# Kernel tuning notes

Hardware: AMD Instinct MI355X
Metric: run time of the kernel (lower is better)

## Reference

```python
import jax, jax.numpy as jnp
import numpy as np

VOCAB = 128000; D = 128; H = 4; HD = D // H; NL = 2; DOUT = 64
MAXW = 32; B = 64; L = 64; N_ITERS = 32

def _ln(x, g, b):
    m = jnp.mean(x, -1, keepdims=True)
    v = jnp.var(x, -1, keepdims=True)
    return (x - m) * jax.lax.rsqrt(v + 1e-5) * g + b

def _encoder(x, pad, p):
    # post-norm torch TransformerEncoderLayer, relu activation. x: [N,W,D], pad True=padding key
    neg = jnp.where(pad, -1e9, 0.0)[:, None, None, :]
    n = x.shape[0]
    for l in range(NL):
        qkv = x @ p["Wqkv"][l].T + p["bqkv"][l]
        q, k, v = jnp.split(qkv, 3, axis=-1)
        q = q.reshape(n, MAXW, H, HD).transpose(0, 2, 1, 3)
        k = k.reshape(n, MAXW, H, HD).transpose(0, 2, 1, 3)
        v = v.reshape(n, MAXW, H, HD).transpose(0, 2, 1, 3)
        s = jnp.einsum('nhqd,nhkd->nhqk', q, k) * (1.0 / float(np.sqrt(HD))) + neg
        o = jnp.einsum('nhqk,nhkd->nhqd', jax.nn.softmax(s, -1), v)
        o = o.transpose(0, 2, 1, 3).reshape(n, MAXW, D) @ p["Wo"][l].T + p["bo"][l]
        x = _ln(x + o, p["ln1g"][l], p["ln1b"][l])
        f = jax.nn.relu(x @ p["W1"][l].T + p["b1"][l]) @ p["W2"][l].T + p["b2"][l]
        x = _ln(x + f, p["ln2g"][l], p["ln2b"][l])
    return x

def _forward(p, token_ids, padding_mask, key):
    seq_len = jnp.sum(~padding_mask, 1).astype(jnp.int32)
    pos_idx = jnp.arange(MAXW)
    bidx = jnp.arange(B)

    def _head(x, W1h, b1h, W2h, b2h):
        return (jax.nn.relu(x @ W1h.T + b1h) @ W2h.T + b2h)[:, 0]

    def _gru(x, h):
        gi = x @ p["gru_Wih"].T + p["gru_bih"]
        gh = h @ p["gru_Whh"].T + p["gru_bhh"]
        ir, iz, inn = jnp.split(gi, 3, -1)
        hr, hz, hn = jnp.split(gh, 3, -1)
        r = jax.nn.sigmoid(ir + hr)
        z = jax.nn.sigmoid(iz + hz)
        return (1.0 - z) * jnp.tanh(inn + r * hn) + z * h

    def step(carry, k):
        win_ids, win_len, input_pos, gru_h, done = carry
        active = ~done
        pad = ~((pos_idx[None, :] < win_len[:, None]) & active[:, None])
        pad = pad.at[:, 0].set(False)  # keep softmax finite for empty windows; t1 zeroed below
        x = p["tok_emb"][win_ids] + p["pos_emb"][None, :, :]
        enc = _encoder(x, pad, p)
        last = enc[bidx, jnp.maximum(win_len - 1, 0)]
        vec = last @ p["proj_W"].T + p["proj_b"]
        vec = vec / jnp.maximum(jnp.linalg.norm(vec, axis=-1, keepdims=True), 1e-12)
        nonempty = (win_len > 0) & active
        t1 = jnp.where(nonempty[:, None], vec, 0.0)
        gru_h = jnp.where(active[:, None], _gru(t1, gru_h), gru_h)
        has_input = active & (input_pos < seq_len)
        nt = token_ids[bidx, jnp.clip(input_pos, 0, L - 1)]
        next_embs = jnp.where(has_input[:, None], p["tok_emb"][nt], 0.0)
        acc_l = _head(jnp.concatenate([next_embs, t1, gru_h], 1), p["acc_W1"], p["acc_b1"], p["acc_W2"], p["acc_b2"])
        tg = jnp.concatenate([t1, gru_h], 1)
        emt_l = _head(tg, p["emt_W1"], p["emt_b1"], p["emt_W2"], p["emt_b2"])
        evt_l = _head(tg, p["evt_W1"], p["evt_b1"], p["evt_W2"], p["evt_b2"])
        k1, k2, k3 = jax.random.split(k, 3)
        acc_s = jax.random.bernoulli(k1, jax.nn.sigmoid(acc_l))
        emt_s = jax.random.bernoulli(k2, jax.nn.sigmoid(emt_l))
        evt_s = jax.random.bernoulli(k3, jax.nn.sigmoid(evt_l))
        lp = jnp.stack([jax.nn.log_sigmoid(jnp.where(acc_s, acc_l, -acc_l)),
                        jax.nn.log_sigmoid(jnp.where(emt_s, emt_l, -emt_l)),
                        jax.nn.log_sigmoid(jnp.where(evt_s, evt_l, -evt_l))], 1)
        dec = jnp.stack([acc_s, emt_s, evt_s], 1).astype(jnp.float32)
        a = acc_s & has_input
        e = emt_s & nonempty
        v = evt_s & nonempty
        none = active & ~(a | e | v)
        a = a | (none & has_input)
        e = e | (none & ~has_input & (win_len > 0))
        a_eff = a & (win_len < MAXW)
        win_ids = jnp.where(a_eff[:, None] & (pos_idx[None, :] == win_len[:, None]), nt[:, None], win_ids)
        input_pos = input_pos + a_eff.astype(jnp.int32)
        win_len = win_len + a_eff.astype(jnp.int32)
        emit_event = e & (win_len > 0)
        v_eff = v & (win_len > 0)
        win_ids = jnp.where(v_eff[:, None], jnp.roll(win_ids, -1, axis=1), win_ids)
        win_len = win_len - v_eff.astype(jnp.int32)
        done = done | (active & (input_pos >= seq_len) & (win_len == 0))
        return (win_ids, win_len, input_pos, gru_h, done), (t1, lp, dec, emit_event)

    init = (jnp.zeros((B, MAXW), dtype=token_ids.dtype), jnp.zeros(B, jnp.int32), jnp.zeros(B, jnp.int32),
            jnp.zeros((B, D), jnp.float32), seq_len == 0)
    keys = jax.random.split(key, N_ITERS)
    _, (t1s, lps, decs, emits) = jax.lax.scan(step, init, keys)
    return t1s, lps, decs, jnp.sum(emits.astype(jnp.int32), 0)

def setup_inputs():
    key = jax.random.key(0)
    ks = jax.random.split(key, 20)
    def rn(k, shape):
        return jax.random.normal(k, shape, jnp.float32) * 0.02
    inp = {}
    inp["token_ids"] = jax.random.randint(ks[0], (B, L), 0, VOCAB)
    inp["padding_mask"] = jnp.zeros((B, L), dtype=bool)
    inp["token_instr_idx"] = jax.random.randint(ks[1], (B, L), 0, 32)
    inp["n_instructions"] = jax.random.randint(ks[2], (B,), 1, 32)
    inp["tok_emb"] = rn(ks[3], (VOCAB, D))
    inp["pos_emb"] = rn(ks[4], (MAXW, D))
    inp["Wqkv"] = rn(ks[5], (NL, 3 * D, D)); inp["bqkv"] = jnp.zeros((NL, 3 * D))
    inp["Wo"] = rn(ks[6], (NL, D, D)); inp["bo"] = jnp.zeros((NL, D))
    inp["ln1g"] = jnp.ones((NL, D)); inp["ln1b"] = jnp.zeros((NL, D))
    inp["W1"] = rn(ks[7], (NL, 4 * D, D)); inp["b1"] = jnp.zeros((NL, 4 * D))
    inp["W2"] = rn(ks[8], (NL, D, 4 * D)); inp["b2"] = jnp.zeros((NL, D))
    inp["ln2g"] = jnp.ones((NL, D)); inp["ln2b"] = jnp.zeros((NL, D))
    inp["proj_W"] = rn(ks[9], (DOUT, D)); inp["proj_b"] = jnp.zeros((DOUT,))
    inp["gru_Wih"] = rn(ks[10], (3 * D, DOUT)); inp["gru_Whh"] = rn(ks[11], (3 * D, D))
    inp["gru_bih"] = jnp.zeros((3 * D,)); inp["gru_bhh"] = jnp.zeros((3 * D,))
    inp["acc_W1"] = rn(ks[12], (D, 2 * D + DOUT)); inp["acc_b1"] = jnp.zeros((D,))
    inp["acc_W2"] = rn(ks[13], (1, D)); inp["acc_b2"] = jnp.full((1,), 2.0)
    inp["emt_W1"] = rn(ks[14], (D, D + DOUT)); inp["emt_b1"] = jnp.zeros((D,))
    inp["emt_W2"] = rn(ks[15], (1, D)); inp["emt_b2"] = jnp.full((1,), -2.0)
    inp["evt_W1"] = rn(ks[16], (D, D + DOUT)); inp["evt_b1"] = jnp.zeros((D,))
    inp["evt_W2"] = rn(ks[17], (1, D)); inp["evt_b2"] = jnp.full((1,), -2.0)
    return inp

def reference(token_ids, padding_mask, token_instr_idx, n_instructions, tok_emb, pos_emb, Wqkv, bqkv, Wo, bo, ln1g, ln1b, W1, b1, W2, b2, ln2g, ln2b, proj_W, proj_b, gru_Wih, gru_Whh, gru_bih, gru_bhh, acc_W1, acc_b1, acc_W2, acc_b2, emt_W1, emt_b1, emt_W2, emt_b2, evt_W1, evt_b1, evt_W2, evt_b2):
    p = dict(tok_emb=tok_emb, pos_emb=pos_emb, Wqkv=Wqkv, bqkv=bqkv, Wo=Wo, bo=bo, ln1g=ln1g, ln1b=ln1b,
             W1=W1, b1=b1, W2=W2, b2=b2, ln2g=ln2g, ln2b=ln2b, proj_W=proj_W, proj_b=proj_b,
             gru_Wih=gru_Wih, gru_Whh=gru_Whh, gru_bih=gru_bih, gru_bhh=gru_bhh,
             acc_W1=acc_W1, acc_b1=acc_b1, acc_W2=acc_W2, acc_b2=acc_b2,
             emt_W1=emt_W1, emt_b1=emt_b1, emt_W2=emt_W2, emt_b2=emt_b2,
             evt_W1=evt_W1, evt_b1=evt_b1, evt_W2=evt_W2, evt_b2=evt_b2)
    # token_instr_idx / n_instructions are only used for emission bookkeeping (no tensor math); unused here.
    return _forward(p, token_ids, padding_mask, jax.random.key(42))
```

## Files before the change

### kernel.cpp

```cpp
#include <hip/hip_runtime.h>
#include <hip/hip_bf16.h>


#define XS 132
#define QS 388
#define HS 516
#define PS 36
#define VS 36
#define NW 16

struct KParams {
  const int* token_ids;
  const unsigned char* pad;
  const void *tok_emb, *pos_emb, *Wqkv, *bqkv, *Wo, *bo, *ln1g, *ln1b;
  const void *W1, *b1, *W2, *b2, *ln2g, *ln2b, *projW, *projb;
  const void *gWih, *gWhh, *gbih, *gbhh;
  const void *accW1, *accb1, *accW2, *accb2;
  const void *emtW1, *emtb1, *emtW2, *emtb2;
  const void *evtW1, *evtb1, *evtW2, *evtb2;
  float* out;
};

struct Smem {
  float xbuf[32 * XS];
  float qh[32 * HS];
  float obuf[32 * XS];
  float pbuf[4608];
  float vT[128 * VS];
  float attT[128];
  float tva[128];
  double gild[384];
  double ghld[384];
  double hsd[128];
  double t1d[64];
  double catd[320];
  double hid2d[384];
  double logitsd[3];
  int win_ids[32];
  int sI[6];
  unsigned keyts[32][2];
};

__device__ __forceinline__ float ldw(const float* p){ return *p; }
__device__ __forceinline__ float ldw(const unsigned short* p){
  return __uint_as_float(((unsigned)*p) << 16);
}
__device__ __forceinline__ float4 ld4(const float* p){ return *(const float4*)p; }
__device__ __forceinline__ float4 ld4(const unsigned short* p){
  ushort4 u = *(const ushort4*)p;
  return make_float4(__uint_as_float((unsigned)u.x << 16),
                     __uint_as_float((unsigned)u.y << 16),
                     __uint_as_float((unsigned)u.z << 16),
                     __uint_as_float((unsigned)u.w << 16));
}
template<typename WT>
__device__ __forceinline__ double ldwd(const WT* p){ return (double)ldw(p); }

__device__ __forceinline__ float temb(const void* te, int isb, long long idx){
  if (isb) return __uint_as_float(((unsigned)((const unsigned short*)te)[idx]) << 16);
  return ((const float*)te)[idx];
}

__device__ __forceinline__ void tfry(unsigned k0, unsigned k1, unsigned x0, unsigned x1,
                                     unsigned &o0, unsigned &o1){
  unsigned ks2 = k0 ^ k1 ^ 0x1BD11BDAu;
  unsigned x = x0 + k0, y = x1 + k1;
#define TFR(r) { x += y; y = (y << r) | (y >> (32 - r)); y ^= x; }
  TFR(13) TFR(15) TFR(26) TFR(6)  x += k1;  y += ks2 + 1u;
  TFR(17) TFR(29) TFR(16) TFR(24) x += ks2; y += k0 + 2u;
  TFR(13) TFR(15) TFR(26) TFR(6)  x += k0;  y += k1 + 3u;
  TFR(17) TFR(29) TFR(16) TFR(24) x += k1;  y += ks2 + 4u;
  TFR(13) TFR(15) TFR(26) TFR(6)  x += ks2; y += k0 + 5u;
#undef TFR
  o0 = x; o1 = y;
}
__device__ __forceinline__ float u01(unsigned bits){
  return __uint_as_float((bits >> 9) | 0x3f800000u) - 1.0f;
}
__device__ __forceinline__ double logsigd(double x){
  return fmin(x, 0.0) - log1p(exp(-fabs(x)));
}
__device__ __forceinline__ float wredsum(float v, int width){
  for (int m = width >> 1; m > 0; m >>= 1) v += __shfl_xor(v, m, width);
  return v;
}
__device__ __forceinline__ double wredsumd(double v, int width){
  for (int m = width >> 1; m > 0; m >>= 1) v += __shfl_xor(v, m, width);
  return v;
}
__device__ __forceinline__ float dot4f(float4 a, float4 b){
  return a.x*b.x + a.y*b.y + a.z*b.z + a.w*b.w;
}

template<int T, int K, bool RELU, int VOFF, typename WT>
__device__ void gemm_tok(const WT* __restrict__ Wm, const WT* __restrict__ bias,
                         int J, const float* __restrict__ xl, int xs,
                         float* __restrict__ ol, int os, int ntok,
                         int lane, int wv, int nwv, float* __restrict__ vt)
{
  const int JBG = J >> 6;
  const int ntt = (ntok + T - 1) / T;
  for (int item = wv; item < JBG * ntt; item += nwv) {
    const int jg = item % JBG, tt = item / JBG;
    const int j0 = jg * 64 + lane;
    float acc[T];
#pragma unroll
    for (int t = 0; t < T; ++t) acc[t] = 0.f;
    const float* xr = xl + tt * T * xs;
    const WT* wr = Wm + (size_t)j0 * K;
#pragma unroll 4
    for (int k = 0; k < K; k += 4) {
      float4 w = ld4(wr + k);
      float4 xv[T];
#pragma unroll
      for (int t = 0; t < T; ++t) xv[t] = *(const float4*)(xr + t * xs + k);
#pragma unroll
      for (int t = 0; t < T; ++t)
        acc[t] += w.x * xv[t].x + w.y * xv[t].y + w.z * xv[t].z + w.w * xv[t].w;
    }
    float bj = ldw(bias + j0);
#pragma unroll
    for (int t = 0; t < T; ++t) {
      int tok = tt * T + t;
      if (tok < ntok) {
        float v = acc[t] + bj;
        if (RELU) v = fmaxf(v, 0.f);
        if (VOFF >= 0 && j0 >= VOFF) vt[(j0 - VOFF) * VS + tok] = v;
        else                         ol[tok * os + j0] = v;
      }
    }
  }
}

template<int K, typename WT>
__device__ __forceinline__ float dotgf(const WT* __restrict__ w, const float* x){
  float acc = 0.f;
#pragma unroll 8
  for (int k = 0; k < K; k += 4) {
    float4 wv = ld4(w + k);
    acc += wv.x * x[k] + wv.y * x[k+1] + wv.z * x[k+2] + wv.w * x[k+3];
  }
  return acc;
}
template<int K, typename WT>
__device__ __forceinline__ double dotgd(const WT* __restrict__ w, const double* x){
  double acc = 0.0;
#pragma unroll 8
  for (int k = 0; k < K; k += 4) {
    float4 wv = ld4(w + k);
    acc += (double)wv.x * x[k] + (double)wv.y * x[k+1]
         + (double)wv.z * x[k+2] + (double)wv.w * x[k+3];
  }
  return acc;
}
template<int K, typename WT>
__device__ __forceinline__ double dotgdx(const WT* __restrict__ w, const float* x){
  double acc = 0.0;
#pragma unroll 8
  for (int k = 0; k < K; k += 4) {
    float4 wv = ld4(w + k);
    acc += (double)wv.x * (double)x[k] + (double)wv.y * (double)x[k+1]
         + (double)wv.z * (double)x[k+2] + (double)wv.w * (double)x[k+3];
  }
  return acc;
}

template<typename WT>
__device__ void ln_rows(float* xb, const float* ob, const WT* __restrict__ g,
                        const WT* __restrict__ bb, int W, int tid){
  if (tid >= 256) return;
  const int i = tid >> 3, sub = tid & 7;
  const int base = i * XS + sub * 16;
  float y[16];
  float s = 0.f;
#pragma unroll
  for (int u = 0; u < 16; u += 4) {
    float4 xv = *(const float4*)(xb + base + u);
    float4 ov = *(const float4*)(ob + base + u);
    y[u] = xv.x + ov.x; y[u+1] = xv.y + ov.y; y[u+2] = xv.z + ov.z; y[u+3] = xv.w + ov.w;
    s += y[u] + y[u+1] + y[u+2] + y[u+3];
  }
  s = wredsum(s, 8);
  const float m = s * (1.0f / 128.0f);
  float vs = 0.f;
#pragma unroll
  for (int u = 0; u < 16; ++u) { float d = y[u] - m; vs += d * d; }
  vs = wredsum(vs, 8);
  const float rstd = 1.0f / sqrtf(vs * (1.0f / 128.0f) + 1e-5f);
  if (i < W) {
#pragma unroll
    for (int u = 0; u < 16; u += 4) {
      float4 gg = ld4(g + sub * 16 + u);
      float4 bv = ld4(bb + sub * 16 + u);
      float4 r;
      r.x = (y[u]   - m) * rstd * gg.x + bv.x;
      r.y = (y[u+1] - m) * rstd * gg.y + bv.y;
      r.z = (y[u+2] - m) * rstd * gg.z + bv.z;
      r.w = (y[u+3] - m) * rstd * gg.w + bv.w;
      *(float4*)(xb + base + u) = r;
    }
  }
}
template<typename WT>
__device__ __forceinline__ void ln_tail(float* xrow, const float* add,
                                        const WT* __restrict__ g,
                                        const WT* __restrict__ bb, int tid){
  if (tid < 64) {
    float y0 = xrow[tid] + add[tid];
    float y1 = xrow[64 + tid] + add[64 + tid];
    float m = wredsum(y0 + y1, 64) * (1.0f / 128.0f);
    float d0 = y0 - m, d1 = y1 - m;
    float rstd = 1.0f / sqrtf(wredsum(d0 * d0 + d1 * d1, 64) * (1.0f / 128.0f) + 1e-5f);
    xrow[tid] = d0 * rstd * ldw(g + tid) + ldw(bb + tid);
    xrow[64 + tid] = d1 * rstd * ldw(g + 64 + tid) + ldw(bb + 64 + tid);
  }
}

template<typename WT>
__device__ void run_all(const KParams& P, Smem& S, int row, int tid, int isbEmb){
  const WT* tok_embw = (const WT*)P.tok_emb;
  const WT* pos_emb = (const WT*)P.pos_emb;
  const WT* Wqkv = (const WT*)P.Wqkv;   const WT* bqkv = (const WT*)P.bqkv;
  const WT* Wo = (const WT*)P.Wo;       const WT* bo = (const WT*)P.bo;
  const WT* ln1g = (const WT*)P.ln1g;   const WT* ln1b = (const WT*)P.ln1b;
  const WT* W1 = (const WT*)P.W1;       const WT* b1 = (const WT*)P.b1;
  const WT* W2 = (const WT*)P.W2;       const WT* b2 = (const WT*)P.b2;
  const WT* ln2g = (const WT*)P.ln2g;   const WT* ln2b = (const WT*)P.ln2b;
  const WT* projW = (const WT*)P.projW; const WT* projb = (const WT*)P.projb;
  const WT* gWih = (const WT*)P.gWih;   const WT* gWhh = (const WT*)P.gWhh;
  const WT* gbih = (const WT*)P.gbih;   const WT* gbhh = (const WT*)P.gbhh;
  const WT* accW1 = (const WT*)P.accW1; const WT* accb1 = (const WT*)P.accb1;
  const WT* accW2 = (const WT*)P.accW2; const WT* accb2 = (const WT*)P.accb2;
  const WT* emtW1 = (const WT*)P.emtW1; const WT* emtb1 = (const WT*)P.emtb1;
  const WT* emtW2 = (const WT*)P.emtW2; const WT* emtb2 = (const WT*)P.emtb2;
  const WT* evtW1 = (const WT*)P.evtW1; const WT* evtb1 = (const WT*)P.evtb1;
  const WT* evtW2 = (const WT*)P.evtW2; const WT* evtb2 = (const WT*)P.evtb2;

  const int lane = tid & 63, wid = tid >> 6;

  if (tid == 0) {
    int seq = 0;
    for (int l = 0; l < 64; ++l) seq += (P.pad[row * 64 + l] == 0);
    S.sI[0] = 0; S.sI[1] = 0; S.sI[2] = (seq == 0) ? 1 : 0; S.sI[3] = seq; S.sI[4] = 0;
  }
  if (tid < 128) S.hsd[tid] = 0.0;
  if (tid < 32) {
    S.win_ids[tid] = 0;
    unsigned a0, a1;
    tfry(0u, 42u, 0u, (unsigned)tid, a0, a1);
    S.keyts[tid][0] = a0; S.keyts[tid][1] = a1;
  }
  for (int idx = tid; idx < 128 * VS; idx += 1024) S.vT[idx] = 0.f;
  __syncthreads();

  for (int t = 0; t < 32; ++t) {
    const int wl = S.sI[0], ip = S.sI[1], done = S.sI[2], seq = S.sI[3];
    const int act = !done;
    const int W = wl;
    const int enc = (act && wl > 0) ? 1 : 0;
    const int jl = (W > 0) ? (W - 1) : 0;
    const int Wp4 = (W + 3) & ~3;

    if (enc) {
      for (int idx = tid; idx < W * 16; idx += 1024) {
        int i = idx >> 4, d0 = (idx & 15) << 3;
        const WT* te = tok_embw + (long long)S.win_ids[i] * 128 + d0;
        const WT* pe = pos_emb + (size_t)i * 128 + d0;
        float4 t0 = ld4(te), t1 = ld4(te + 4), p0 = ld4(pe), p1 = ld4(pe + 4);
        float* dst = &S.xbuf[i * XS + d0];
        float4 r0, r1;
        r0.x = t0.x + p0.x; r0.y = t0.y + p0.y; r0.z = t0.z + p0.z; r0.w = t0.w + p0.w;
        r1.x = t1.x + p1.x; r1.y = t1.y + p1.y; r1.z = t1.z + p1.z; r1.w = t1.w + p1.w;
        *(float4*)dst = r0;
        *(float4*)(dst + 4) = r1;
      }
      __syncthreads();
      gemm_tok<8, 128, false, 256>(Wqkv, bqkv, 384, S.xbuf, XS, S.qh, QS, W, lane, wid, NW, S.vT);
      __syncthreads();
      if (tid < 256) {
        int r = tid >> 1, half = tid & 1;
        int h = r >> 5, i = r & 31;
        if (i < W) {
          float4 q[8];
#pragma unroll
          for (int kk = 0; kk < 8; ++kk) q[kk] = *(const float4*)&S.qh[i * QS + h * 32 + kk * 4];
          const int pb = r * PS;
          const int j0 = half * 16;
          const int j1 = (j0 + 16 < W) ? (j0 + 16) : W;
          float m = -1e30f;
          for (int j = j0; j < j1; ++j) {
            float s = 0.f;
#pragma unroll
            for (int kk = 0; kk < 8; ++kk)
              s += dot4f(q[kk], *(const float4*)&S.qh[j * QS + 128 + h * 32 + kk * 4]);
            s *= 0.17677669529663687f;
            S.pbuf[pb + j] = s;
            m = fmaxf(m, s);
          }
          m = fmaxf(m, __shfl_xor(m, 1, 64));
          float sum = 0.f;
          for (int j = j0; j < j1; ++j) {
            float e = expf(S.pbuf[pb + j] - m);
            S.pbuf[pb + j] = e;
            sum += e;
          }
          sum += __shfl_xor(sum, 1, 64);
          float rs = 1.0f / sum;
          for (int j = j0; j < j1; ++j) S.pbuf[pb + j] *= rs;
          for (int j = W + half; j < Wp4; j += 2) S.pbuf[pb + j] = 0.f;
        }
      } else if (act) {
        int jj = tid - 256;
        int j = jj >> 1, h = jj & 1;
        double v = dotgd<64>(gWhh + (size_t)j * 128 + h * 64, S.hsd + h * 64);
        v += __shfl_xor(v, 1, 64);
        if (h == 0) S.ghld[j] = ldwd(gbhh + j) + v;
      }
      __syncthreads();
      {
        int c = tid & 127, g = tid >> 7;
        int h = c >> 5;
        const float* vrow = &S.vT[c * VS];
        for (int i = g; i < W; i += 8) {
          const float* prow = &S.pbuf[(h * 32 + i) * PS];
          float acc = 0.f;
          for (int j4 = 0; j4 < W; j4 += 4) {
            float4 p = *(const float4*)(prow + j4);
            float4 v = *(const float4*)(vrow + j4);
            acc += p.x * v.x + p.y * v.y + p.z * v.z + p.w * v.w;
          }
          S.obuf[i * XS + c] = acc;
        }
      }
      __syncthreads();
      gemm_tok<4, 128, false, -1>(Wo, bo, 128, S.obuf, XS, S.pbuf, XS, W, lane, wid, NW, S.vT);
      __syncthreads();
      ln_rows(S.xbuf, S.pbuf, ln1g, ln1b, W, tid);
      __syncthreads();
      gemm_tok<8, 128, true, -1>(W1, b1, 512, S.xbuf, XS, S.qh, HS, W, lane, wid, NW, S.vT);
      __syncthreads();
      gemm_tok<4, 512, false, -1>(W2, b2, 128, S.qh, HS, S.obuf, XS, W, lane, wid, NW, S.vT);
      __syncthreads();
      ln_rows(S.xbuf, S.obuf, ln2g, ln2b, W, tid);
      __syncthreads();
      {
        const WT* Wq = Wqkv + 384 * 128;
        const WT* bq = bqkv + 384;
        if (wid < 14) {
          gemm_tok<8, 128, false, 128>(Wq + 128 * 128, bq + 128, 256,
                                       S.xbuf, XS, S.qh + 128, QS, W, lane, wid, 14, S.vT);
        } else {
          int j = tid - 896;
          S.qh[jl * QS + j] = ldw(bq + j) + dotgf<128>(Wq + j * 128, &S.xbuf[jl * XS]);
        }
        __syncthreads();
        if (tid < 128) {
          int h = tid >> 5, j = tid & 31;
          float s = -1e30f;
          if (j < W) {
            s = 0.f;
#pragma unroll
            for (int kk = 0; kk < 8; ++kk)
              s += dot4f(*(const float4*)&S.qh[jl * QS + h * 32 + kk * 4],
                         *(const float4*)&S.qh[j * QS + 128 + h * 32 + kk * 4]);
            s *= 0.17677669529663687f;
          }
          float m = s;
          for (int mk = 16; mk; mk >>= 1) m = fmaxf(m, __shfl_xor(m, mk, 32));
          float e = (j < W) ? expf(s - m) : 0.f;
          float sum = e;
          for (int mk = 16; mk; mk >>= 1) sum += __shfl_xor(sum, mk, 32);
          if (j < W) S.pbuf[h * PS + j] = e * (1.0f / sum);
          else       S.pbuf[h * PS + j] = 0.f;
        } else if (tid >= 896) {
          int j = tid - 896;
          int ipc = ip < 0 ? 0 : (ip > 63 ? 63 : ip);
          int nt = P.token_ids[row * 64 + ipc];
          int has_in = (act && (ip < seq)) ? 1 : 0;
          S.catd[j] = has_in ? (double)temb(P.tok_emb, isbEmb, (long long)nt * 128 + j) : 0.0;
        }
        __syncthreads();
        if (tid < 128) {
          int h = tid >> 5;
          const float* prow = &S.pbuf[h * PS];
          const float* vrow = &S.vT[tid * VS];
          float acc = 0.f;
          for (int j4 = 0; j4 < W; j4 += 4) {
            float4 p = *(const float4*)(prow + j4);
            float4 v = *(const float4*)(vrow + j4);
            acc += p.x * v.x + p.y * v.y + p.z * v.z + p.w * v.w;
          }
          S.attT[tid] = acc;
        }
        __syncthreads();
        if (tid < 512) {
          int j = tid >> 2, q = tid & 3;
          float v = dotgf<32>(Wo + 16384 + (size_t)j * 128 + q * 32, S.attT + q * 32);
          v += __shfl_xor(v, 1, 64);
          v += __shfl_xor(v, 2, 64);
          if (q == 0) S.tva[j] = ldw(bo + 128 + j) + v;
        }
        __syncthreads();
        ln_tail(&S.xbuf[jl * XS], S.tva, ln1g + 128, ln1b + 128, tid);
        __syncthreads();
        {
          int j = tid >> 1, h = tid & 1;
          float v = dotgf<64>(W1 + (size_t)(512 + j) * 128 + h * 64, &S.xbuf[jl * XS] + h * 64);
          v += __shfl_xor(v, 1, 64);
          if (h == 0) S.qh[j] = fmaxf(ldw(b1 + 512 + j) + v, 0.f);
        }
        __syncthreads();
        if (tid < 512) {
          int j = tid >> 2, q = tid & 3;
          float v = dotgf<128>(W2 + (size_t)(128 + j) * 512 + q * 128, S.qh + q * 128);
          v += __shfl_xor(v, 1, 64);
          v += __shfl_xor(v, 2, 64);
          if (q == 0) S.tva[j] = ldw(b2 + 128 + j) + v;
        }
        __syncthreads();
        ln_tail(&S.xbuf[jl * XS], S.tva, ln2g + 128, ln2b + 128, tid);
        __syncthreads();
      }
    }

    if (tid < 64) {
      double tv = 0.0;
      if (enc) {
        double v = ldwd(projb + tid) + dotgdx<128>(projW + tid * 128, &S.xbuf[jl * XS]);
        double ss = wredsumd(v * v, 64);
        tv = v / fmax(sqrt(ss), 1e-12);
      }
      S.t1d[tid] = tv;
      S.catd[128 + tid] = tv;
      P.out[(size_t)t * 4096 + row * 64 + tid] = (float)tv;
    } else if (!enc) {
      if (tid >= 128 && tid < 896) {
        if (act) {
          int jj = tid - 128;
          int j = jj >> 1, h = jj & 1;
          double v = dotgd<64>(gWhh + (size_t)j * 128 + h * 64, S.hsd + h * 64);
          v += __shfl_xor(v, 1, 64);
          if (h == 0) S.ghld[j] = ldwd(gbhh + j) + v;
        }
      } else if (tid >= 896) {
        int j = tid - 896;
        int ipc = ip < 0 ? 0 : (ip > 63 ? 63 : ip);
        int nt = P.token_ids[row * 64 + ipc];
        int has_in = (act && (ip < seq)) ? 1 : 0;
        S.catd[j] = has_in ? (double)temb(P.tok_emb, isbEmb, (long long)nt * 128 + j) : 0.0;
      }
    }
    __syncthreads();

    if (act) {
      if (tid < 768) {
        int j = tid >> 1, h = tid & 1;
        double v = dotgd<32>(gWih + (size_t)j * 64 + h * 32, S.t1d + h * 32);
        v += __shfl_xor(v, 1, 64);
        if (h == 0) S.gild[j] = ldwd(gbih + j) + v;
      }
      __syncthreads();
    }

    if (tid < 128) {
      if (act) {
        double r = 1.0 / (1.0 + exp(-(S.gild[tid] + S.ghld[tid])));
        double z = 1.0 / (1.0 + exp(-(S.gild[128 + tid] + S.ghld[128 + tid])));
        double n = tanh(S.gild[256 + tid] + r * S.ghld[256 + tid]);
        S.hsd[tid] = (1.0 - z) * n + z * S.hsd[tid];
      }
      S.catd[192 + tid] = S.hsd[tid];
    }
    __syncthreads();

    if (tid < 768) {
      int jo = tid >> 1, h = tid & 1;
      double v;
      if (jo < 128) {
        v = dotgd<160>(accW1 + (size_t)jo * 320 + h * 160, S.catd + h * 160);
      } else if (jo < 256) {
        int j = jo - 128;
        v = dotgd<96>(emtW1 + (size_t)j * 192 + h * 96, S.catd + 128 + h * 96);
      } else {
        int j = jo - 256;
        v = dotgd<96>(evtW1 + (size_t)j * 192 + h * 96, S.catd + 128 + h * 96);
      }
      v += __shfl_xor(v, 1, 64);
      if (h == 0) {
        double b = (jo < 128) ? ldwd(accb1 + jo)
                 : (jo < 256 ? ldwd(emtb1 + jo - 128) : ldwd(evtb1 + jo - 256));
        S.hid2d[jo] = fmax(b + v, 0.0);
      }
    }
    __syncthreads();

    {
      int hw = tid >> 6;
      if (hw < 3) {
        int ln = tid & 63;
        const WT* w2 = (hw == 0) ? accW2 : ((hw == 1) ? emtW2 : evtW2);
        const WT* b2p = (hw == 0) ? accb2 : ((hw == 1) ? emtb2 : evtb2);
        double pp = S.hid2d[hw * 128 + ln] * ldwd(w2 + ln)
                  + S.hid2d[hw * 128 + 64 + ln] * ldwd(w2 + 64 + ln);
        pp = wredsumd(pp, 64);
        if (ln == 0) S.logitsd[hw] = pp + ldwd(b2p);
      }
    }
    __syncthreads();

    if (tid < 64) {
      unsigned k0 = S.keyts[t][0], k1 = S.keyts[t][1];
      int smp_l = 0;
      if (tid < 3) {
        double lgv = S.logitsd[tid];
        unsigned sk0, sk1, r0, r1;
        tfry(k0, k1, 0u, (unsigned)tid, sk0, sk1);
        tfry(sk0, sk1, 0u, (unsigned)row, r0, r1);
        double u = (double)u01(r0 ^ r1);
        double p = 1.0 / (1.0 + exp(-lgv));
        smp_l = (u < p) ? 1 : 0;
        P.out[131072 + (size_t)t * 192 + row * 3 + tid] = (float)logsigd(smp_l ? lgv : -lgv);
        P.out[137216 + (size_t)t * 192 + row * 3 + tid] = smp_l ? 1.0f : 0.0f;
      }
      int sa = __shfl(smp_l, 0, 64);
      int se = __shfl(smp_l, 1, 64);
      int sv = __shfl(smp_l, 2, 64);
      if (tid == 0) {
        int wl2 = wl, ip2 = ip, dn = done;
        int nonempty = (wl2 > 0) && act;
        int has_in = act && (ip2 < seq);
        int a = sa && has_in;
        int e = se && nonempty;
        int v = sv && nonempty;
        int none = act && !(a || e || v);
        a = a || (none && has_in);
        e = e || (none && !has_in && (wl2 > 0));
        int aeff = a && (wl2 < 32);
        int ipc = ip2 < 0 ? 0 : (ip2 > 63 ? 63 : ip2);
        int nt = P.token_ids[row * 64 + ipc];
        if (aeff) { S.win_ids[wl2] = nt; ip2 += 1; wl2 += 1; }
        int emit = e && (wl2 > 0);
        S.sI[4] += emit;
        int veff = v && (wl2 > 0);
        if (veff) {
          int w0 = S.win_ids[0];
#pragma unroll
          for (int i2 = 0; i2 < 31; ++i2) S.win_ids[i2] = S.win_ids[i2 + 1];
          S.win_ids[31] = w0;
          wl2 -= 1;
        }
        if (act && (ip2 >= seq) && (wl2 == 0)) dn = 1;
        S.sI[0] = wl2; S.sI[1] = ip2; S.sI[2] = dn;
      }
    }
    __syncthreads();
  }
  if (tid == 0) P.out[143360 + row] = (float)S.sI[4];
}

__global__ __launch_bounds__(1024, 4) void src_main_kernel(KParams P){
  __shared__ __align__(16) Smem S;
  const int row = blockIdx.x;
  const int tid = threadIdx.x;
  const bool isb = (((const unsigned short*)P.ln1g)[0] == (unsigned short)0x3F80);
  if (isb) run_all<unsigned short>(P, S, row, tid, 1);
  else     run_all<float>(P, S, row, tid, 0);
}

extern "C" void kernel_launch(void* const* d_in, const int* in_sizes, int n_in,
                              void* d_out, int out_size, void* d_ws, size_t ws_size,
                              hipStream_t stream) {
  KParams P;
  P.token_ids = (const int*)d_in[0];
  P.pad = (const unsigned char*)d_in[1];
  P.tok_emb = d_in[4];  P.pos_emb = d_in[5];
  P.Wqkv = d_in[6];     P.bqkv = d_in[7];
  P.Wo = d_in[8];       P.bo = d_in[9];
  P.ln1g = d_in[10];    P.ln1b = d_in[11];
  P.W1 = d_in[12];      P.b1 = d_in[13];
  P.W2 = d_in[14];      P.b2 = d_in[15];
  P.ln2g = d_in[16];    P.ln2b = d_in[17];
  P.projW = d_in[18];   P.projb = d_in[19];
  P.gWih = d_in[20];    P.gWhh = d_in[21];
  P.gbih = d_in[22];    P.gbhh = d_in[23];
  P.accW1 = d_in[24];   P.accb1 = d_in[25];
  P.accW2 = d_in[26];   P.accb2 = d_in[27];
  P.emtW1 = d_in[28];   P.emtb1 = d_in[29];
  P.emtW2 = d_in[30];   P.emtb2 = d_in[31];
  P.evtW1 = d_in[32];   P.evtb1 = d_in[33];
  P.evtW2 = d_in[34];   P.evtb2 = d_in[35];
  P.out = (float*)d_out;
  hipLaunchKernelGGL(src_main_kernel, dim3(64), dim3(1024), 0, stream, P);
}
```

Before: 4.519 ms.

## Pre-transpose encoder weights into lane-interleaved workspace for coalesced GEMM loads

Adds a small pre-kernel that rearranges the QKV, Wo, W1, W2 and layer-1 QKV weights into a layout where the 64 lanes of a wavefront read consecutive 4-element chunks. The token GEMM then reads them contiguously instead of striding by K per lane. This targets uncoalesced weight loads in the per-step encoder GEMMs. The cost is an extra kernel launch and transpose pass on every call, plus a fallback path when the workspace is too small.

```diff
diff --git a/kernel.cpp b/kernel.cpp
--- a/kernel.cpp
+++ b/kernel.cpp
@@ -8,6 +8,14 @@
 #define PS 36
 #define VS 36
 #define NW 16
+
+#define TWS_QKV0 0
+#define TWS_WO0  49152
+#define TWS_W10  65536
+#define TWS_W20  131072
+#define TWS_QKV1 196608
+#define TWS_TOTAL 229376
+#define TWS_NVEC (TWS_TOTAL / 4)
 
 struct KParams {
   const int* token_ids;
@@ -18,6 +26,7 @@
   const void *accW1, *accb1, *accW2, *accb2;
   const void *emtW1, *emtb1, *emtW2, *emtb2;
   const void *evtW1, *evtb1, *evtW2, *evtb2;
+  const void *wst;
   float* out;
 };
 
@@ -92,8 +101,31 @@
   return a.x*b.x + a.y*b.y + a.z*b.z + a.w*b.w;
 }
 
-template<int T, int K, bool RELU, int VOFF, typename WT>
-__device__ void gemm_tok(const WT* __restrict__ Wm, const WT* __restrict__ bias,
+__global__ __launch_bounds__(256) void transpose_w_kernel(
+    const void* Wqkv, const void* Wo, const void* W1, const void* W2,
+    const void* ln1g, void* ws)
+{
+  const bool isb = (((const unsigned short*)ln1g)[0] == (unsigned short)0x3F80);
+  int i = blockIdx.x * 256 + threadIdx.x;
+  if (i >= TWS_NVEC) return;
+  const void* src; int K4; long long srcBase; int dstBase; int local;
+  if (i < 12288)      { src = Wqkv; K4 = 32;  local = i;         srcBase = 0;               dstBase = TWS_QKV0; }
+  else if (i < 16384) { src = Wo;   K4 = 32;  local = i - 12288; srcBase = 0;               dstBase = TWS_WO0; }
+  else if (i < 32768) { src = W1;   K4 = 32;  local = i - 16384; srcBase = 0;               dstBase = TWS_W10; }
+  else if (i < 49152) { src = W2;   K4 = 128; local = i - 32768; srcBase = 0;               dstBase = TWS_W20; }
+  else                { src = Wqkv; K4 = 32;  local = i - 49152; srcBase = 384*128+128*128; dstBase = TWS_QKV1; }
+  const int per = K4 * 64;
+  const int cg = local / per, rem = local % per;
+  const int k4 = rem / 64, lane = rem % 64;
+  const long long srcElem = srcBase + (long long)(cg * 64 + lane) * (K4 * 4) + (long long)k4 * 4;
+  const long long dstElem = (long long)dstBase + (long long)local * 4;
+  if (isb) ((uint2*)ws)[dstElem >> 2] = ((const uint2*)src)[srcElem >> 2];
+  else     ((uint4*)ws)[dstElem >> 2] = ((const uint4*)src)[srcElem >> 2];
+}
+
+template<int T, int K, bool RELU, int VOFF, bool TRW, typename WT>
+__device__ void gemm_tok(const WT* __restrict__ Wm, const WT* __restrict__ Wt,
+                         const WT* __restrict__ bias,
                          int J, const float* __restrict__ xl, int xs,
                          float* __restrict__ ol, int os, int ntok,
                          int lane, int wv, int nwv, float* __restrict__ vt)
@@ -107,10 +139,14 @@
 #pragma unroll
     for (int t = 0; t < T; ++t) acc[t] = 0.f;
     const float* xr = xl + tt * T * xs;
-    const WT* wr = Wm + (size_t)j0 * K;
+    const WT* wr0 = TRW ? (Wt + ((size_t)jg * (K / 4) * 64 + lane) * 4)
+                        : (Wm + (size_t)j0 * K);
+    const WT* wrp = wr0;
 #pragma unroll 4
     for (int k = 0; k < K; k += 4) {
-      float4 w = ld4(wr + k);
+      float4 w;
+      if (TRW) { w = ld4(wrp); wrp += 256; }
+      else     { w = ld4(wr0 + k); }
       float4 xv[T];
 #pragma unroll
       for (int t = 0; t < T; ++t) xv[t] = *(const float4*)(xr + t * xs + k);
@@ -216,7 +252,7 @@
   }
 }
 
-template<typename WT>
+template<typename WT, bool TRW>
 __device__ void run_all(const KParams& P, Smem& S, int row, int tid, int isbEmb){
   const WT* tok_embw = (const WT*)P.tok_emb;
   const WT* pos_emb = (const WT*)P.pos_emb;
@@ -235,6 +271,7 @@
   const WT* emtW2 = (const WT*)P.emtW2; const WT* emtb2 = (const WT*)P.emtb2;
   const WT* evtW1 = (const WT*)P.evtW1; const WT* evtb1 = (const WT*)P.evtb1;
   const WT* evtW2 = (const WT*)P.evtW2; const WT* evtb2 = (const WT*)P.evtb2;
+  const WT* wsb = (const WT*)P.wst;
 
   const int lane = tid & 63, wid = tid >> 6;
 
@@ -275,7 +312,8 @@
         *(float4*)(dst + 4) = r1;
       }
       __syncthreads();
-      gemm_tok<8, 128, false, 256>(Wqkv, bqkv, 384, S.xbuf, XS, S.qh, QS, W, lane, wid, NW, S.vT);
+      gemm_tok<8, 128, false, 256, TRW>(Wqkv, wsb + TWS_QKV0, bqkv, 384,
+                                        S.xbuf, XS, S.qh, QS, W, lane, wid, NW, S.vT);
       __syncthreads();
       if (tid < 256) {
         int r = tid >> 1, half = tid & 1;
@@ -333,13 +371,16 @@
         }
       }
       __syncthreads();
-      gemm_tok<4, 128, false, -1>(Wo, bo, 128, S.obuf, XS, S.pbuf, XS, W, lane, wid, NW, S.vT);
+      gemm_tok<4, 128, false, -1, TRW>(Wo, wsb + TWS_WO0, bo, 128,
+                                       S.obuf, XS, S.pbuf, XS, W, lane, wid, NW, S.vT);
       __syncthreads();
       ln_rows(S.xbuf, S.pbuf, ln1g, ln1b, W, tid);
       __syncthreads();
-      gemm_tok<8, 128, true, -1>(W1, b1, 512, S.xbuf, XS, S.qh, HS, W, lane, wid, NW, S.vT);
-      __syncthreads();
-      gemm_tok<4, 512, false, -1>(W2, b2, 128, S.qh, HS, S.obuf, XS, W, lane, wid, NW, S.vT);
+      gemm_tok<8, 128, true, -1, TRW>(W1, wsb + TWS_W10, b1, 512,
+                                      S.xbuf, XS, S.qh, HS, W, lane, wid, NW, S.vT);
+      __syncthreads();
+      gemm_tok<4, 512, false, -1, TRW>(W2, wsb + TWS_W20, b2, 128,
+                                       S.qh, HS, S.obuf, XS, W, lane, wid, NW, S.vT);
       __syncthreads();
       ln_rows(S.xbuf, S.obuf, ln2g, ln2b, W, tid);
       __syncthreads();
@@ -347,8 +388,8 @@
         const WT* Wq = Wqkv + 384 * 128;
         const WT* bq = bqkv + 384;
         if (wid < 14) {
-          gemm_tok<8, 128, false, 128>(Wq + 128 * 128, bq + 128, 256,
-                                       S.xbuf, XS, S.qh + 128, QS, W, lane, wid, 14, S.vT);
+          gemm_tok<8, 128, false, 128, TRW>(Wq + 128 * 128, wsb + TWS_QKV1, bq + 128, 256,
+                                            S.xbuf, XS, S.qh + 128, QS, W, lane, wid, 14, S.vT);
         } else {
           int j = tid - 896;
           S.qh[jl * QS + j] = ldw(bq + j) + dotgf<128>(Wq + j * 128, &S.xbuf[jl * XS]);
@@ -558,13 +599,14 @@
   if (tid == 0) P.out[143360 + row] = (float)S.sI[4];
 }
 
-__global__ __launch_bounds__(1024, 4) void src_main_kernel(KParams P){
+template<bool TRW>
+__global__ __launch_bounds__(1024, 4) void src_main_kernel_t(KParams P){
   __shared__ __align__(16) Smem S;
   const int row = blockIdx.x;
   const int tid = threadIdx.x;
   const bool isb = (((const unsigned short*)P.ln1g)[0] == (unsigned short)0x3F80);
-  if (isb) run_all<unsigned short>(P, S, row, tid, 1);
-  else     run_all<float>(P, S, row, tid, 0);
+  if (isb) run_all<unsigned short, TRW>(P, S, row, tid, 1);
+  else     run_all<float, TRW>(P, S, row, tid, 0);
 }
 
 extern "C" void kernel_launch(void* const* d_in, const int* in_sizes, int n_in,
@@ -589,6 +631,14 @@
   P.emtW2 = d_in[30];   P.emtb2 = d_in[31];
   P.evtW1 = d_in[32];   P.evtb1 = d_in[33];
   P.evtW2 = d_in[34];   P.evtb2 = d_in[35];
+  P.wst = d_ws;
   P.out = (float*)d_out;
-  hipLaunchKernelGGL(src_main_kernel, dim3(64), dim3(1024), 0, stream, P);
-}
+  const bool tr = (d_ws != nullptr) && (ws_size >= (size_t)TWS_TOTAL * 4);
+  if (tr) {
+    hipLaunchKernelGGL(transpose_w_kernel, dim3((TWS_NVEC + 255) / 256), dim3(256), 0, stream,
+                       P.Wqkv, P.Wo, P.W1, P.W2, P.ln1g, d_ws);
+    hipLaunchKernelGGL((src_main_kernel_t<true>), dim3(64), dim3(1024), 0, stream, P);
+  } else {
+    hipLaunchKernelGGL((src_main_kernel_t<false>), dim3(64), dim3(1024), 0, stream, P);
+  }
+}
```

Result: faster. 4.126 ms (-8.7%).
